# Kernel tuning notes

Measured on AMD Instinct MI355X. Metric: run time of the kernel, lower is better.

Reference implementation:

```python
import jax, jax.numpy as jnp
import numpy as np

BETA = 0.25


def setup_inputs() -> dict:
    key = jax.random.key(0)
    k1, k2 = jax.random.split(key)
    x = jax.random.normal(k1, (32, 32, 32, 256), dtype=jnp.float32)
    codebook = jax.random.normal(k2, (1024, 256), dtype=jnp.float32)
    return {"x": x, "codebook": codebook}


def reference(x, codebook):
    D = codebook.shape[1]
    z_fla = x.reshape(-1, D)  # [N, D]
    # squared euclidean distances [N, K]
    dis = (jnp.sum(z_fla ** 2, axis=1, keepdims=True)
           + jnp.sum(codebook ** 2, axis=1)
           - 2.0 * jnp.matmul(z_fla, codebook.T))
    min_encoding_indices = jnp.argmin(dis, axis=1)  # [N] int
    z_q = codebook[min_encoding_indices].reshape(x.shape)
    loss = (jnp.mean((jax.lax.stop_gradient(z_q) - x) ** 2)
            + BETA * jnp.mean((z_q - jax.lax.stop_gradient(x)) ** 2))
    z_q = x + jax.lax.stop_gradient(z_q - x)  # straight-through
    # faithful to source: mean of the index values, then "perplexity" formula
    e_min = jnp.mean(min_encoding_indices.astype(jnp.float32), axis=0)
    perplexity = jnp.exp(-jnp.sum(e_min * jnp.log(e_min + 1e-10)))
    return (loss, z_q, perplexity, min_encoding_indices)
```

## Files before the change

kernel.cpp:

```cpp
#include <hip/hip_runtime.h>
#include <cmath>

#define NROWS 32768
#define DDIM  256
#define KCB   1024

constexpr float TAU = 0.25f;
constexpr int BSTR = 264;

typedef _Float16 half8 __attribute__((ext_vector_type(8)));
typedef float floatx4 __attribute__((ext_vector_type(4)));

__global__ void init_kernel(double* __restrict__ sumsq,
                            int* __restrict__ sumidx,
                            unsigned* __restrict__ done) {
  *sumsq = 0.0;
  *sumidx = 0;
  *done = 0u;
}

__global__ __launch_bounds__(512, 2) void fused_kernel(
    const float* __restrict__ x,
    const float* __restrict__ cb,
    float* __restrict__ zq_out,
    float* __restrict__ idx_out,
    float* __restrict__ out_loss,
    float* __restrict__ out_perp,
    double* __restrict__ sumsq,
    int* __restrict__ sumidx,
    unsigned* __restrict__ done) {
  __shared__ __align__(16) _Float16 bs[2][64 * BSTR];
  __shared__ float cn_lds[KCB];
  __shared__ int   bidx[128];
  __shared__ int   bidx2[128];
  __shared__ float m2s[128];
  __shared__ float m3s[128];
  __shared__ __align__(16) float xrow[DDIM];
  __shared__ int   plist[128];
  __shared__ int   flist[128];
  __shared__ int   npair, nfull;
  __shared__ float wred[8];
  __shared__ double rv[8];
  __shared__ int    ri[8];

  const int tid = threadIdx.x;
  const int lane = tid & 63;
  const int w = tid >> 6;
  const int q = lane >> 4;
  const int tx = lane & 15;
  const int row0 = blockIdx.x * 128;

  half8 a_hi[8], a_lo[8];
  {
    const float* xp = x + (size_t)(row0 + w * 16 + tx) * DDIM + q * 8;
    #pragma unroll
    for (int s = 0; s < 8; ++s) {
      float4 v0 = *(const float4*)(xp + s * 32);
      float4 v1 = *(const float4*)(xp + s * 32 + 4);
      half8 h, l;
      _Float16 t;
      t = (_Float16)v0.x; h[0] = t; l[0] = (_Float16)(v0.x - (float)t);
      t = (_Float16)v0.y; h[1] = t; l[1] = (_Float16)(v0.y - (float)t);
      t = (_Float16)v0.z; h[2] = t; l[2] = (_Float16)(v0.z - (float)t);
      t = (_Float16)v0.w; h[3] = t; l[3] = (_Float16)(v0.w - (float)t);
      t = (_Float16)v1.x; h[4] = t; l[4] = (_Float16)(v1.x - (float)t);
      t = (_Float16)v1.y; h[5] = t; l[5] = (_Float16)(v1.y - (float)t);
      t = (_Float16)v1.z; h[6] = t; l[6] = (_Float16)(v1.z - (float)t);
      t = (_Float16)v1.w; h[7] = t; l[7] = (_Float16)(v1.w - (float)t);
      a_hi[s] = h; a_lo[s] = l;
    }
  }
  if (tid == 0) { npair = 0; nfull = 0; }

  float4 vld[8];
  auto load_stage = [&](int ct) {
    #pragma unroll
    for (int i = 0; i < 4; ++i) {
      int p = tid + 512 * i;
      const float* src = cb + (size_t)ct * 16384 + (size_t)p * 8;
      vld[2 * i]     = *(const float4*)src;
      vld[2 * i + 1] = *(const float4*)(src + 4);
    }
  };
  auto write_stage = [&](int buf, int ct) {
    #pragma unroll
    for (int i = 0; i < 4; ++i) {
      int p = tid + 512 * i;
      int e = p >> 5, c = p & 31;
      float4 v0 = vld[2 * i], v1 = vld[2 * i + 1];
      half8 h;
      h[0] = (_Float16)v0.x; h[1] = (_Float16)v0.y;
      h[2] = (_Float16)v0.z; h[3] = (_Float16)v0.w;
      h[4] = (_Float16)v1.x; h[5] = (_Float16)v1.y;
      h[6] = (_Float16)v1.z; h[7] = (_Float16)v1.w;
      *(half8*)&bs[buf][e * BSTR + c * 8] = h;
      double s = (double)v0.x * v0.x + (double)v0.y * v0.y
               + (double)v0.z * v0.z + (double)v0.w * v0.w
               + (double)v1.x * v1.x + (double)v1.y * v1.y
               + (double)v1.z * v1.z + (double)v1.w * v1.w;
      #pragma unroll
      for (int off = 16; off; off >>= 1) s += __shfl_down(s, off, 32);
      if ((tid & 31) == 0) cn_lds[ct * 64 + e] = (float)s;
    }
  };

  float v1[4], v2[4], v3[4];
  int i1[4], i2[4];
  #pragma unroll
  for (int r = 0; r < 4; ++r) {
    v1[r] = INFINITY; v2[r] = INFINITY; v3[r] = INFINITY; i1[r] = 0; i2[r] = 0;
  }

  load_stage(0);
  for (int st = 0; st < 16; ++st) {
    const int buf = st & 1;
    write_stage(buf, st);
    __syncthreads();
    if (st + 1 < 16) load_stage(st + 1);

    floatx4 ahh[4], alh[4];
    #pragma unroll
    for (int ci = 0; ci < 4; ++ci) {
      ahh[ci] = (floatx4){0.f, 0.f, 0.f, 0.f};
      alh[ci] = (floatx4){0.f, 0.f, 0.f, 0.f};
    }

    #pragma unroll
    for (int s = 0; s < 8; ++s) {
      #pragma unroll
      for (int ci = 0; ci < 4; ++ci) {
        half8 bh = *(const half8*)&bs[buf][(ci * 16 + tx) * BSTR + (s * 4 + q) * 8];
        ahh[ci] = __builtin_amdgcn_mfma_f32_16x16x32_f16(a_hi[s], bh, ahh[ci], 0, 0, 0);
        alh[ci] = __builtin_amdgcn_mfma_f32_16x16x32_f16(a_lo[s], bh, alh[ci], 0, 0, 0);
      }
    }

    #pragma unroll
    for (int ci = 0; ci < 4; ++ci) {
      int col = st * 64 + ci * 16 + tx;
      float cnv = cn_lds[col];
      #pragma unroll
      for (int r = 0; r < 4; ++r) {
        float dot = ahh[ci][r] + alh[ci][r];
        float dist = cnv - 2.f * dot;
        if (dist < v1[r]) {
          v3[r] = v2[r]; v2[r] = v1[r]; i2[r] = i1[r];
          v1[r] = dist; i1[r] = col;
        } else if (dist < v2[r]) {
          v3[r] = v2[r]; v2[r] = dist; i2[r] = col;
        } else if (dist < v3[r]) {
          v3[r] = dist;
        }
      }
    }
  }

  #pragma unroll
  for (int off = 8; off; off >>= 1) {
    #pragma unroll
    for (int r = 0; r < 4; ++r) {
      float ov1 = __shfl_down(v1[r], off, 16);
      int   oi1 = __shfl_down(i1[r], off, 16);
      float ov2 = __shfl_down(v2[r], off, 16);
      int   oi2 = __shfl_down(i2[r], off, 16);
      float ov3 = __shfl_down(v3[r], off, 16);
      bool takeo = (ov1 < v1[r]) || (ov1 == v1[r] && oi1 < i1[r]);
      float n1v = takeo ? ov1 : v1[r];
      int   n1i = takeo ? oi1 : i1[r];
      float l1 = takeo ? v1[r] : v2[r];
      int   l1i = takeo ? i1[r] : i2[r];
      float l2 = takeo ? v2[r] : v3[r];
      float r1 = takeo ? ov2 : ov1;
      int   r1i = takeo ? oi2 : oi1;
      float r2 = takeo ? ov3 : ov2;
      bool t2 = (r1 < l1) || (r1 == l1 && r1i < l1i);
      float n2v = t2 ? r1 : l1;
      int   n2i = t2 ? r1i : l1i;
      float n3v = t2 ? fminf(r2, l1) : fminf(l2, r1);
      v1[r] = n1v; i1[r] = n1i; v2[r] = n2v; i2[r] = n2i; v3[r] = n3v;
    }
  }
  if (tx == 0) {
    #pragma unroll
    for (int r = 0; r < 4; ++r) {
      int R = w * 16 + q * 4 + r;
      bidx[R]  = i1[r];
      bidx2[R] = i2[r];
      m2s[R] = v2[r] - v1[r];
      m3s[R] = v3[r] - v1[r];
    }
  }
  __syncthreads();

  if (tid < 128) {
    if (m3s[tid] < TAU) {
      int p = atomicAdd(&nfull, 1);
      flist[p] = tid;
    } else if (m2s[tid] < TAU) {
      int p = atomicAdd(&npair, 1);
      plist[p] = tid;
    }
  }
  __syncthreads();

  for (int f = 0; f < nfull; ++f) {
    int r = flist[f];
    if (tid < 64) {
      float4 v = *(const float4*)(x + (size_t)(row0 + r) * DDIM + tid * 4);
      xrow[tid * 4 + 0] = v.x; xrow[tid * 4 + 1] = v.y;
      xrow[tid * 4 + 2] = v.z; xrow[tid * 4 + 3] = v.w;
    }
    __syncthreads();
    double bd = 1e300; int bi = 0;
    #pragma unroll
    for (int j = 0; j < 2; ++j) {
      int c = 2 * tid + j;
      const float* cp = cb + (size_t)c * DDIM;
      double s0 = 0.0, s1 = 0.0, s2 = 0.0, s3 = 0.0;
      for (int d = 0; d < DDIM; d += 4) {
        float4 cv = *(const float4*)(cp + d);
        float4 xv = *(const float4*)&xrow[d];
        double d0 = (double)xv.x - (double)cv.x; s0 = fma(d0, d0, s0);
        double d1 = (double)xv.y - (double)cv.y; s1 = fma(d1, d1, s1);
        double d2 = (double)xv.z - (double)cv.z; s2 = fma(d2, d2, s2);
        double d3 = (double)xv.w - (double)cv.w; s3 = fma(d3, d3, s3);
      }
      double s = (s0 + s1) + (s2 + s3);
      if (s < bd) { bd = s; bi = c; }
    }
    #pragma unroll
    for (int off = 32; off; off >>= 1) {
      double ov = __shfl_down(bd, off);
      int oi = __shfl_down(bi, off);
      if (ov < bd || (ov == bd && oi < bi)) { bd = ov; bi = oi; }
    }
    if (lane == 0) { rv[w] = bd; ri[w] = bi; }
    __syncthreads();
    if (tid == 0) {
      double bv = rv[0]; int bix = ri[0];
      for (int ww = 1; ww < 8; ++ww)
        if (rv[ww] < bv || (rv[ww] == bv && ri[ww] < bix)) { bv = rv[ww]; bix = ri[ww]; }
      bidx[r] = bix;
    }
    __syncthreads();
  }

  for (int f = w; f < npair; f += 8) {
    int r = plist[f];
    int cA = bidx[r], cB = bidx2[r];
    int c = (lane >= 32) ? cB : cA;
    int ld = lane & 31;
    const float* xp = x  + (size_t)(row0 + r) * DDIM + ld * 8;
    const float* cp = cb + (size_t)c * DDIM + ld * 8;
    double s = 0.0;
    #pragma unroll
    for (int j = 0; j < 8; j += 4) {
      float4 xv = *(const float4*)(xp + j);
      float4 cv = *(const float4*)(cp + j);
      double d0 = (double)xv.x - (double)cv.x; s = fma(d0, d0, s);
      double d1 = (double)xv.y - (double)cv.y; s = fma(d1, d1, s);
      double d2 = (double)xv.z - (double)cv.z; s = fma(d2, d2, s);
      double d3 = (double)xv.w - (double)cv.w; s = fma(d3, d3, s);
    }
    #pragma unroll
    for (int off = 16; off; off >>= 1) s += __shfl_xor(s, off);
    double dA = __shfl(s, 0), dB = __shfl(s, 32);
    if (lane == 0) {
      bool takeB = (dB < dA) || (dB == dA && cB < cA);
      bidx[r] = takeB ? cB : cA;
    }
  }
  __syncthreads();

  if (tid < 128) idx_out[row0 + tid] = (float)bidx[tid];

  float lsum = 0.f;
  #pragma unroll 4
  for (int it = 0; it < 16; ++it) {
    int g = tid + 512 * it;
    int r = g >> 6;
    int c4 = (g & 63) << 2;
    int k = bidx[r] & (KCB - 1);
    float4 cv = *(const float4*)(cb + (size_t)k * DDIM + c4);
    float4 xv = *(const float4*)(x + (size_t)(row0 + r) * DDIM + c4);
    float d0 = cv.x - xv.x, d1 = cv.y - xv.y, d2 = cv.z - xv.z, d3 = cv.w - xv.w;
    lsum = fmaf(d0, d0, lsum); lsum = fmaf(d1, d1, lsum);
    lsum = fmaf(d2, d2, lsum); lsum = fmaf(d3, d3, lsum);
    *(float4*)(zq_out + (size_t)(row0 + r) * DDIM + c4) = cv;
  }
  #pragma unroll
  for (int off = 32; off; off >>= 1) lsum += __shfl_down(lsum, off);
  if (lane == 0) wred[w] = lsum;
  __syncthreads();
  if (tid == 0) {
    double ls = 0.0;
    #pragma unroll
    for (int ww = 0; ww < 8; ++ww) ls += (double)wred[ww];
    atomicAdd(sumsq, ls);
    int si = 0;
    #pragma unroll 8
    for (int r = 0; r < 128; ++r) si += bidx[r] & (KCB - 1);
    atomicAdd(sumidx, si);

    __threadfence();
    unsigned prev = atomicAdd(done, 1u);
    if (prev == gridDim.x - 1) {
      __threadfence();
      double ss = atomicAdd(sumsq, 0.0);
      int    sidx = atomicAdd(sumidx, 0);
      double loss = 1.25 * ss / 8388608.0;
      double e_min = (double)sidx / 32768.0;
      double perp = exp(-e_min * log(e_min + 1e-10));
      *out_loss = (float)loss;
      *out_perp = (float)perp;
    }
  }
}

extern "C" void kernel_launch(void* const* d_in, const int* in_sizes, int n_in,
                              void* d_out, int out_size, void* d_ws, size_t ws_size,
                              hipStream_t stream) {
  const float* x  = (const float*)d_in[0];
  const float* cb = (const float*)d_in[1];
  float* out = (float*)d_out;
  float* out_loss = out;
  float* out_zq   = out + 1;
  float* out_perp = out + 1 + 8388608;
  float* out_idx  = out + 2 + 8388608;

  double*   sumsq  = (double*)d_ws;
  int*      sumidx = (int*)((char*)d_ws + 8);
  unsigned* done   = (unsigned*)((char*)d_ws + 12);

  hipLaunchKernelGGL(init_kernel, dim3(1), dim3(1), 0, stream,
                     sumsq, sumidx, done);
  hipLaunchKernelGGL(fused_kernel, dim3(NROWS / 128), dim3(512), 0, stream,
                     x, cb, out_zq, out_idx, out_loss, out_perp,
                     sumsq, sumidx, done);
}
```

Measured before the change: 191.6 us.

## Move full-rescan rows to a global cleanup kernel and precompute codebook norms

Rows whose top-3 distance gaps are ambiguous are no longer rescanned serially inside each fused block. They are appended to a global list and rescanned exactly in fp64 by a separate cleanup kernel spread over many blocks, which patches the index, z_q, loss and index sum by deltas. Codebook squared norms move into a small prep kernel instead of being recomputed by every block during staging. This removes per-block tail imbalance and redundant norm work, at the cost of two extra launches and global atomics.

```diff
diff --git a/kernel.cpp b/kernel.cpp
--- a/kernel.cpp
+++ b/kernel.cpp
@@ -11,37 +11,41 @@
 typedef _Float16 half8 __attribute__((ext_vector_type(8)));
 typedef float floatx4 __attribute__((ext_vector_type(4)));
 
-__global__ void init_kernel(double* __restrict__ sumsq,
-                            int* __restrict__ sumidx,
-                            unsigned* __restrict__ done) {
-  *sumsq = 0.0;
-  *sumidx = 0;
-  *done = 0u;
+__global__ void init_kernel(double* __restrict__ sumsq, int* __restrict__ sumidx,
+                            unsigned* __restrict__ done2, int* __restrict__ nfull) {
+  *sumsq = 0.0; *sumidx = 0; *done2 = 0u; *nfull = 0;
+}
+
+__global__ __launch_bounds__(64) void prep_kernel(const float* __restrict__ cb,
+                                                  float* __restrict__ cn) {
+  const int k = blockIdx.x, lane = threadIdx.x;
+  float4 v = *(const float4*)(cb + (size_t)k * DDIM + lane * 4);
+  double s = (double)v.x * v.x + (double)v.y * v.y
+           + (double)v.z * v.z + (double)v.w * v.w;
+  #pragma unroll
+  for (int off = 32; off; off >>= 1) s += __shfl_down(s, off);
+  if (lane == 0) cn[k] = (float)s;
 }
 
 __global__ __launch_bounds__(512, 2) void fused_kernel(
     const float* __restrict__ x,
     const float* __restrict__ cb,
+    const float* __restrict__ cn,
     float* __restrict__ zq_out,
     float* __restrict__ idx_out,
-    float* __restrict__ out_loss,
-    float* __restrict__ out_perp,
     double* __restrict__ sumsq,
     int* __restrict__ sumidx,
-    unsigned* __restrict__ done) {
+    int* __restrict__ nfull_g,
+    int* __restrict__ glist) {
   __shared__ __align__(16) _Float16 bs[2][64 * BSTR];
   __shared__ float cn_lds[KCB];
   __shared__ int   bidx[128];
   __shared__ int   bidx2[128];
   __shared__ float m2s[128];
   __shared__ float m3s[128];
-  __shared__ __align__(16) float xrow[DDIM];
   __shared__ int   plist[128];
-  __shared__ int   flist[128];
-  __shared__ int   npair, nfull;
+  __shared__ int   npair;
   __shared__ float wred[8];
-  __shared__ double rv[8];
-  __shared__ int    ri[8];
 
   const int tid = threadIdx.x;
   const int lane = tid & 63;
@@ -70,7 +74,9 @@
       a_hi[s] = h; a_lo[s] = l;
     }
   }
-  if (tid == 0) { npair = 0; nfull = 0; }
+  cn_lds[tid] = cn[tid];
+  cn_lds[tid + 512] = cn[tid + 512];
+  if (tid == 0) npair = 0;
 
   float4 vld[8];
   auto load_stage = [&](int ct) {
@@ -82,7 +88,7 @@
       vld[2 * i + 1] = *(const float4*)(src + 4);
     }
   };
-  auto write_stage = [&](int buf, int ct) {
+  auto write_stage = [&](int buf) {
     #pragma unroll
     for (int i = 0; i < 4; ++i) {
       int p = tid + 512 * i;
@@ -94,13 +100,6 @@
       h[4] = (_Float16)v1.x; h[5] = (_Float16)v1.y;
       h[6] = (_Float16)v1.z; h[7] = (_Float16)v1.w;
       *(half8*)&bs[buf][e * BSTR + c * 8] = h;
-      double s = (double)v0.x * v0.x + (double)v0.y * v0.y
-               + (double)v0.z * v0.z + (double)v0.w * v0.w
-               + (double)v1.x * v1.x + (double)v1.y * v1.y
-               + (double)v1.z * v1.z + (double)v1.w * v1.w;
-      #pragma unroll
-      for (int off = 16; off; off >>= 1) s += __shfl_down(s, off, 32);
-      if ((tid & 31) == 0) cn_lds[ct * 64 + e] = (float)s;
     }
   };
 
@@ -114,7 +113,7 @@
   load_stage(0);
   for (int st = 0; st < 16; ++st) {
     const int buf = st & 1;
-    write_stage(buf, st);
+    write_stage(buf);
     __syncthreads();
     if (st + 1 < 16) load_stage(st + 1);
 
@@ -194,56 +193,14 @@
 
   if (tid < 128) {
     if (m3s[tid] < TAU) {
-      int p = atomicAdd(&nfull, 1);
-      flist[p] = tid;
+      int p = atomicAdd(nfull_g, 1);
+      glist[p] = row0 + tid;
     } else if (m2s[tid] < TAU) {
       int p = atomicAdd(&npair, 1);
       plist[p] = tid;
     }
   }
   __syncthreads();
-
-  for (int f = 0; f < nfull; ++f) {
-    int r = flist[f];
-    if (tid < 64) {
-      float4 v = *(const float4*)(x + (size_t)(row0 + r) * DDIM + tid * 4);
-      xrow[tid * 4 + 0] = v.x; xrow[tid * 4 + 1] = v.y;
-      xrow[tid * 4 + 2] = v.z; xrow[tid * 4 + 3] = v.w;
-    }
-    __syncthreads();
-    double bd = 1e300; int bi = 0;
-    #pragma unroll
-    for (int j = 0; j < 2; ++j) {
-      int c = 2 * tid + j;
-      const float* cp = cb + (size_t)c * DDIM;
-      double s0 = 0.0, s1 = 0.0, s2 = 0.0, s3 = 0.0;
-      for (int d = 0; d < DDIM; d += 4) {
-        float4 cv = *(const float4*)(cp + d);
-        float4 xv = *(const float4*)&xrow[d];
-        double d0 = (double)xv.x - (double)cv.x; s0 = fma(d0, d0, s0);
-        double d1 = (double)xv.y - (double)cv.y; s1 = fma(d1, d1, s1);
-        double d2 = (double)xv.z - (double)cv.z; s2 = fma(d2, d2, s2);
-        double d3 = (double)xv.w - (double)cv.w; s3 = fma(d3, d3, s3);
-      }
-      double s = (s0 + s1) + (s2 + s3);
-      if (s < bd) { bd = s; bi = c; }
-    }
-    #pragma unroll
-    for (int off = 32; off; off >>= 1) {
-      double ov = __shfl_down(bd, off);
-      int oi = __shfl_down(bi, off);
-      if (ov < bd || (ov == bd && oi < bi)) { bd = ov; bi = oi; }
-    }
-    if (lane == 0) { rv[w] = bd; ri[w] = bi; }
-    __syncthreads();
-    if (tid == 0) {
-      double bv = rv[0]; int bix = ri[0];
-      for (int ww = 1; ww < 8; ++ww)
-        if (rv[ww] < bv || (rv[ww] == bv && ri[ww] < bix)) { bv = rv[ww]; bix = ri[ww]; }
-      bidx[r] = bix;
-    }
-    __syncthreads();
-  }
 
   for (int f = w; f < npair; f += 8) {
     int r = plist[f];
@@ -301,9 +258,90 @@
     #pragma unroll 8
     for (int r = 0; r < 128; ++r) si += bidx[r] & (KCB - 1);
     atomicAdd(sumidx, si);
-
+  }
+}
+
+__global__ __launch_bounds__(256) void cleanup_kernel(
+    const float* __restrict__ x,
+    const float* __restrict__ cb,
+    float* __restrict__ zq_out,
+    float* __restrict__ idx_out,
+    float* __restrict__ out_loss,
+    float* __restrict__ out_perp,
+    double* __restrict__ sumsq,
+    int* __restrict__ sumidx,
+    const int* __restrict__ nfull_g,
+    const int* __restrict__ glist,
+    unsigned* __restrict__ done2) {
+  __shared__ __align__(16) float xr[DDIM];
+  __shared__ double rv[4];
+  __shared__ int    ri[4];
+  __shared__ double dold_s;
+  __shared__ int    kstar_s;
+
+  const int tid = threadIdx.x;
+  const int lane = tid & 63;
+  const int w = tid >> 6;
+  const int nitems = *nfull_g;
+
+  for (int it = blockIdx.x; it < nitems; it += gridDim.x) {
+    int row = glist[it];
+    int kold = (int)idx_out[row];
+    __syncthreads();
+    if (tid < 64) {
+      float4 v = *(const float4*)(x + (size_t)row * DDIM + tid * 4);
+      xr[tid * 4 + 0] = v.x; xr[tid * 4 + 1] = v.y;
+      xr[tid * 4 + 2] = v.z; xr[tid * 4 + 3] = v.w;
+    }
+    __syncthreads();
+    double bd = 1e300; int bi = 0;
+    #pragma unroll
+    for (int j = 0; j < 4; ++j) {
+      int c = tid * 4 + j;
+      const float* cp = cb + (size_t)c * DDIM;
+      double s0 = 0.0, s1 = 0.0, s2 = 0.0, s3 = 0.0;
+      for (int d = 0; d < DDIM; d += 4) {
+        float4 cv = *(const float4*)(cp + d);
+        float4 xv = *(const float4*)&xr[d];
+        double d0 = (double)xv.x - (double)cv.x; s0 = fma(d0, d0, s0);
+        double d1 = (double)xv.y - (double)cv.y; s1 = fma(d1, d1, s1);
+        double d2 = (double)xv.z - (double)cv.z; s2 = fma(d2, d2, s2);
+        double d3 = (double)xv.w - (double)cv.w; s3 = fma(d3, d3, s3);
+      }
+      double s = (s0 + s1) + (s2 + s3);
+      if (s < bd) { bd = s; bi = c; }
+      if (c == kold) dold_s = s;
+    }
+    #pragma unroll
+    for (int off = 32; off; off >>= 1) {
+      double ov = __shfl_down(bd, off);
+      int oi = __shfl_down(bi, off);
+      if (ov < bd || (ov == bd && oi < bi)) { bd = ov; bi = oi; }
+    }
+    if (lane == 0) { rv[w] = bd; ri[w] = bi; }
+    __syncthreads();
+    if (tid == 0) {
+      double bv = rv[0]; int bix = ri[0];
+      #pragma unroll
+      for (int ww = 1; ww < 4; ++ww)
+        if (rv[ww] < bv || (rv[ww] == bv && ri[ww] < bix)) { bv = rv[ww]; bix = ri[ww]; }
+      if (bix != kold) {
+        idx_out[row] = (float)bix;
+        atomicAdd(sumsq, bv - dold_s);
+        atomicAdd(sumidx, bix - kold);
+      }
+      kstar_s = bix;
+    }
+    __syncthreads();
+    int kst = kstar_s;
+    if (kst != kold)
+      zq_out[(size_t)row * DDIM + tid] = cb[(size_t)kst * DDIM + tid];
+  }
+
+  __syncthreads();
+  if (tid == 0) {
     __threadfence();
-    unsigned prev = atomicAdd(done, 1u);
+    unsigned prev = atomicAdd(done2, 1u);
     if (prev == gridDim.x - 1) {
       __threadfence();
       double ss = atomicAdd(sumsq, 0.0);
@@ -330,11 +368,17 @@
 
   double*   sumsq  = (double*)d_ws;
   int*      sumidx = (int*)((char*)d_ws + 8);
-  unsigned* done   = (unsigned*)((char*)d_ws + 12);
+  unsigned* done2  = (unsigned*)((char*)d_ws + 12);
+  int*      nfull  = (int*)((char*)d_ws + 16);
+  float*    cn     = (float*)((char*)d_ws + 64);
+  int*      glist  = (int*)((char*)d_ws + 8192);
 
   hipLaunchKernelGGL(init_kernel, dim3(1), dim3(1), 0, stream,
-                     sumsq, sumidx, done);
+                     sumsq, sumidx, done2, nfull);
+  hipLaunchKernelGGL(prep_kernel, dim3(KCB), dim3(64), 0, stream, cb, cn);
   hipLaunchKernelGGL(fused_kernel, dim3(NROWS / 128), dim3(512), 0, stream,
+                     x, cb, cn, out_zq, out_idx, sumsq, sumidx, nfull, glist);
+  hipLaunchKernelGGL(cleanup_kernel, dim3(256), dim3(256), 0, stream,
                      x, cb, out_zq, out_idx, out_loss, out_perp,
-                     sumsq, sumidx, done);
-}
+                     sumsq, sumidx, nfull, glist, done2);
+}
```

New measurement: 181.7 us. -5.2%, faster.
